# Optimization experiments

Hardware: AMD Instinct MI355X
Metric: run time of the kernel (lower is better)

The kernel has to match this reference:

```python
import jax, jax.numpy as jnp
import numpy as np


def _dsepconv(inp, vert, horiz, offx, offy, mask):
    # inp: [B,C,H,W]; vert/horiz: [B,F,H,W]; offx/offy/mask: [B,F*F,H,W]
    B, C, H, W = inp.shape
    F = vert.shape[1]
    FF = F * F
    dt = inp.dtype
    k = jnp.arange(FF)
    ki = (k // F).astype(dt)   # vertical tap index i
    kj = (k % F).astype(dt)    # horizontal tap index j
    half = jnp.asarray((F - 1) / 2.0, dt)
    ys = jnp.arange(H, dtype=dt)
    xs = jnp.arange(W, dtype=dt)
    # per-pixel deformable sample positions, [B,FF,H,W]
    py = offy + ys[None, None, :, None] + (ki - half)[None, :, None, None]
    px = offx + xs[None, None, None, :] + (kj - half)[None, :, None, None]
    py = jnp.clip(py, 0.0, H - 1)
    px = jnp.clip(px, 0.0, W - 1)
    y0f = jnp.floor(py)
    x0f = jnp.floor(px)
    wy = py - y0f   # bilinear fractional weights
    wx = px - x0f
    y0 = y0f.astype(jnp.int32)
    x0 = x0f.astype(jnp.int32)
    y1 = jnp.minimum(y0 + 1, H - 1)
    x1 = jnp.minimum(x0 + 1, W - 1)

    inp_flat = inp.reshape(B, C, H * W)

    def gather(yi, xi):
        # flat spatial gather per batch element -> [B,C,FF,H,W]
        idx = (yi * W + xi).reshape(B, FF * H * W)
        g = jax.vmap(lambda im, ix: im[:, ix])(inp_flat, idx)
        return g.reshape(B, C, FF, H, W)

    g00 = gather(y0, x0)
    g01 = gather(y0, x1)
    g10 = gather(y1, x0)
    g11 = gather(y1, x1)
    wy_ = wy[:, None]  # [B,1,FF,H,W]
    wx_ = wx[:, None]
    samp = (g00 * (1 - wy_) * (1 - wx_)
            + g01 * (1 - wy_) * wx_
            + g10 * wy_ * (1 - wx_)
            + g11 * wy_ * wx_)  # [B,C,FF,H,W]
    # separable mask-weighted tap weights: vert[i]*horiz[j]*mask[k]
    wtap = vert[:, k // F] * horiz[:, k % F] * mask  # [B,FF,H,W]
    return jnp.einsum('bkhw,bckhw->bchw', wtap, samp)


def setup_inputs() -> dict:
    key = jax.random.key(0)
    ks = jax.random.split(key, 6)
    B, C, H, W, F = 4, 3, 384, 384, 5
    return {
        'tensorInput': jax.random.normal(ks[0], (B, C, H, W), jnp.float32),
        'tensorVertical': jax.random.uniform(ks[1], (B, F, H, W), jnp.float32),
        'tensorHorizontal': jax.random.uniform(ks[2], (B, F, H, W), jnp.float32),
        'tensorOffsetX': jax.random.normal(ks[3], (B, F * F, H, W), jnp.float32),
        'tensorOffsetY': jax.random.normal(ks[4], (B, F * F, H, W), jnp.float32),
        'tensorMask': jax.random.uniform(ks[5], (B, F * F, H, W), jnp.float32),
    }


def reference(tensorInput, tensorVertical, tensorHorizontal, tensorOffsetX, tensorOffsetY, tensorMask):
    return _dsepconv(tensorInput, tensorVertical, tensorHorizontal,
                     tensorOffsetX, tensorOffsetY, tensorMask)
```

## Files before the change

### kernel.cpp

```cpp
#include <hip/hip_runtime.h>
#include <hip/hip_fp16.h>

#define BB 4
#define CC 3
#define HH 384
#define WW 384
#define FF 5
#define KK 25
#define HW (HH*WW)
#define WP 192
#define TOT (BB*HH*WP)

#define TX 64
#define TY 8

typedef float fx2 __attribute__((ext_vector_type(2)));

__device__ __forceinline__ fx2 nt_load2(const float* p) {
    return __builtin_nontemporal_load((const fx2*)p);
}

__device__ __forceinline__ uint2 pack_px(float c0, float c1, float c2) {
    __half2 h01 = __floats2half2_rn(c0, c1);
    uint2 r;
    r.x = *(const unsigned int*)&h01;
    r.y = (unsigned int)__half_as_ushort(__float2half_rn(c2));
    return r;
}

__global__ __launch_bounds__(256) void pack_kernel(
    const float* __restrict__ inp, uint4* __restrict__ tab)
{
    int t = blockIdx.x * blockDim.x + threadIdx.x;
    if (t >= TOT) return;
    int j = t % WP;
    int y = (t / WP) % HH;
    int b = t / (WP * HH);
    int p0 = 2 * j, p1 = 2 * j + 1, p2 = min(2 * j + 2, WW - 1);
    const float* b0 = inp + (((size_t)b * CC + 0) * HH + y) * WW;
    const float* b1 = inp + (((size_t)b * CC + 1) * HH + y) * WW;
    const float* b2 = inp + (((size_t)b * CC + 2) * HH + y) * WW;
    uint2 q0 = pack_px(b0[p0], b1[p0], b2[p0]);
    uint2 q1 = pack_px(b0[p1], b1[p1], b2[p1]);
    uint2 q2 = pack_px(b0[p2], b1[p2], b2[p2]);
    tab[t]       = make_uint4(q0.x, q0.y, q1.x, q1.y);
    tab[TOT + t] = make_uint4(q1.x, q1.y, q2.x, q2.y);
}

__device__ __forceinline__ void unpack_pair(uint4 r,
    float& lo0, float& lo1, float& lo2, float& hi0, float& hi1, float& hi2)
{
    float2 lo01 = __half22float2(*(const __half2*)&r.x);
    float2 hi01 = __half22float2(*(const __half2*)&r.z);
    lo0 = lo01.x; lo1 = lo01.y;
    hi0 = hi01.x; hi1 = hi01.y;
    lo2 = __half2float(*(const __half*)&r.y);
    hi2 = __half2float(*(const __half*)&r.w);
}

__global__ __launch_bounds__(256) void dsepconv_kernel(
    const uint4* __restrict__ tab,
    const float* __restrict__ vert,
    const float* __restrict__ horiz,
    const float* __restrict__ offx,
    const float* __restrict__ offy,
    const float* __restrict__ mask,
    float* __restrict__ out)
{
    int tx = threadIdx.x & 31;
    int ty = threadIdx.x >> 5;
    int xb = blockIdx.x * TX + tx * 2;
    int y  = blockIdx.y * TY + ty;
    int b  = blockIdx.z;
    int planeoff = y * WW + xb;

    fx2 v2[FF], h2[FF];
#pragma unroll
    for (int f = 0; f < FF; ++f) {
        v2[f] = nt_load2(vert  + (b * FF + f) * HW + planeoff);
        h2[f] = nt_load2(horiz + (b * FF + f) * HW + planeoff);
    }

    const uint4* tb = tab + (size_t)b * (HH * WP);

    float acc[2][3] = {{0.f,0.f,0.f},{0.f,0.f,0.f}};
    const float fy = (float)y;

    for (int ki = 0; ki < FF; ++ki) {
        float dy = fy + (float)(ki - 2);
        const float* ox_p = offx + (size_t)(b * KK + ki * FF) * HW + planeoff;
        const float* oy_p = offy + (size_t)(b * KK + ki * FF) * HW + planeoff;
        const float* m_p  = mask + (size_t)(b * KK + ki * FF) * HW + planeoff;
#pragma unroll
        for (int kj = 0; kj < FF; ++kj) {
            fx2 ox2 = nt_load2(ox_p + kj * HW);
            fx2 oy2 = nt_load2(oy_p + kj * HW);
            fx2 m2  = nt_load2(m_p  + kj * HW);
#pragma unroll
            for (int p = 0; p < 2; ++p) {
                float wt = v2[ki][p] * h2[kj][p] * m2[p];
                float py = oy2[p] + dy;
                float px = ox2[p] + (float)(xb + p + kj - 2);
                py = fminf(fmaxf(py, 0.f), (float)(HH - 1));
                px = fminf(fmaxf(px, 0.f), (float)(WW - 1));
                float y0f = floorf(py);
                float x0f = floorf(px);
                float wy = py - y0f;
                float wx = px - x0f;
                int y0 = (int)y0f;
                int x0 = (int)x0f;
                int y1 = min(y0 + 1, HH - 1);

                int j    = x0 >> 1;
                const uint4* tbs = tb + ((x0 & 1) ? TOT : 0);
                uint4 r0 = tbs[y0 * WP + j];
                uint4 r1 = tbs[y1 * WP + j];

                float a00,a01,a02,b00,b01,b02;
                float a10,a11,a12,b10,b11,b12;
                unpack_pair(r0, a00,a01,a02, b00,b01,b02);
                unpack_pair(r1, a10,a11,a12, b10,b11,b12);

                float w00 = (1.f - wy) * (1.f - wx);
                float w01 = (1.f - wy) * wx;
                float w10 = wy * (1.f - wx);
                float w11 = wy * wx;

                acc[p][0] += wt * (a00*w00 + b00*w01 + a10*w10 + b10*w11);
                acc[p][1] += wt * (a01*w00 + b01*w01 + a11*w10 + b11*w11);
                acc[p][2] += wt * (a02*w00 + b02*w01 + a12*w10 + b12*w11);
            }
        }
    }

#pragma unroll
    for (int c = 0; c < CC; ++c) {
        fx2 o; o.x = acc[0][c]; o.y = acc[1][c];
        *(fx2*)(out + ((size_t)b * CC + c) * HW + planeoff) = o;
    }
}

extern "C" void kernel_launch(void* const* d_in, const int* in_sizes, int n_in,
                              void* d_out, int out_size, void* d_ws, size_t ws_size,
                              hipStream_t stream) {
    const float* inp   = (const float*)d_in[0];
    const float* vert  = (const float*)d_in[1];
    const float* horiz = (const float*)d_in[2];
    const float* offx  = (const float*)d_in[3];
    const float* offy  = (const float*)d_in[4];
    const float* mask  = (const float*)d_in[5];
    float* out = (float*)d_out;
    uint4* tab = (uint4*)d_ws;

    {
        pack_kernel<<<(TOT + 255) / 256, 256, 0, stream>>>(inp, tab);
    }
    {
        dim3 grid(WW / TX, HH / TY, BB);
        dsepconv_kernel<<<grid, 256, 0, stream>>>(
            tab, vert, horiz, offx, offy, mask, out);
    }
}
```

Baseline: 219.3 us.

## Map one pixel per thread with fully unrolled tap loops and batched loads

```diff
diff --git a/kernel.cpp b/kernel.cpp
--- a/kernel.cpp
+++ b/kernel.cpp
@@ -12,12 +12,12 @@
 #define TOT (BB*HH*WP)
 
 #define TX 64
-#define TY 8
+#define TY 4
 
 typedef float fx2 __attribute__((ext_vector_type(2)));
 
-__device__ __forceinline__ fx2 nt_load2(const float* p) {
-    return __builtin_nontemporal_load((const fx2*)p);
+__device__ __forceinline__ float nt_load(const float* p) {
+    return __builtin_nontemporal_load(p);
 }
 
 __device__ __forceinline__ uint2 pack_px(float c0, float c1, float c2) {
@@ -36,13 +36,18 @@
     int j = t % WP;
     int y = (t / WP) % HH;
     int b = t / (WP * HH);
-    int p0 = 2 * j, p1 = 2 * j + 1, p2 = min(2 * j + 2, WW - 1);
+    int p0 = 2 * j;
+    int p2 = min(2 * j + 2, WW - 1);
     const float* b0 = inp + (((size_t)b * CC + 0) * HH + y) * WW;
     const float* b1 = inp + (((size_t)b * CC + 1) * HH + y) * WW;
     const float* b2 = inp + (((size_t)b * CC + 2) * HH + y) * WW;
-    uint2 q0 = pack_px(b0[p0], b1[p0], b2[p0]);
-    uint2 q1 = pack_px(b0[p1], b1[p1], b2[p1]);
-    uint2 q2 = pack_px(b0[p2], b1[p2], b2[p2]);
+    fx2 a0 = *(const fx2*)(b0 + p0);
+    fx2 a1 = *(const fx2*)(b1 + p0);
+    fx2 a2 = *(const fx2*)(b2 + p0);
+    float c0 = b0[p2], c1 = b1[p2], c2 = b2[p2];
+    uint2 q0 = pack_px(a0.x, a1.x, a2.x);
+    uint2 q1 = pack_px(a0.y, a1.y, a2.y);
+    uint2 q2 = pack_px(c0, c1, c2);
     tab[t]       = make_uint4(q0.x, q0.y, q1.x, q1.y);
     tab[TOT + t] = make_uint4(q1.x, q1.y, q2.x, q2.y);
 }
@@ -58,7 +63,7 @@
     hi2 = __half2float(*(const __half*)&r.w);
 }
 
-__global__ __launch_bounds__(256) void dsepconv_kernel(
+__global__ __launch_bounds__(256, 6) void dsepconv_kernel(
     const uint4* __restrict__ tab,
     const float* __restrict__ vert,
     const float* __restrict__ horiz,
@@ -67,77 +72,79 @@
     const float* __restrict__ mask,
     float* __restrict__ out)
 {
-    int tx = threadIdx.x & 31;
-    int ty = threadIdx.x >> 5;
-    int xb = blockIdx.x * TX + tx * 2;
+    int tx = threadIdx.x & 63;
+    int ty = threadIdx.x >> 6;
+    int x  = blockIdx.x * TX + tx;
     int y  = blockIdx.y * TY + ty;
     int b  = blockIdx.z;
-    int planeoff = y * WW + xb;
+    int planeoff = y * WW + x;
 
-    fx2 v2[FF], h2[FF];
+    float v[FF], h[FF];
 #pragma unroll
     for (int f = 0; f < FF; ++f) {
-        v2[f] = nt_load2(vert  + (b * FF + f) * HW + planeoff);
-        h2[f] = nt_load2(horiz + (b * FF + f) * HW + planeoff);
+        v[f] = nt_load(vert  + (b * FF + f) * HW + planeoff);
+        h[f] = nt_load(horiz + (b * FF + f) * HW + planeoff);
     }
 
     const uint4* tb = tab + (size_t)b * (HH * WP);
 
-    float acc[2][3] = {{0.f,0.f,0.f},{0.f,0.f,0.f}};
+    float acc0 = 0.f, acc1 = 0.f, acc2 = 0.f;
     const float fy = (float)y;
 
+#pragma unroll
     for (int ki = 0; ki < FF; ++ki) {
-        float dy = fy + (float)(ki - 2);
+        const float dy = fy + (float)(ki - 2);
         const float* ox_p = offx + (size_t)(b * KK + ki * FF) * HW + planeoff;
         const float* oy_p = offy + (size_t)(b * KK + ki * FF) * HW + planeoff;
         const float* m_p  = mask + (size_t)(b * KK + ki * FF) * HW + planeoff;
+
+        float oxv[FF], oyv[FF], mv[FF];
 #pragma unroll
         for (int kj = 0; kj < FF; ++kj) {
-            fx2 ox2 = nt_load2(ox_p + kj * HW);
-            fx2 oy2 = nt_load2(oy_p + kj * HW);
-            fx2 m2  = nt_load2(m_p  + kj * HW);
+            oxv[kj] = nt_load(ox_p + kj * HW);
+            oyv[kj] = nt_load(oy_p + kj * HW);
+            mv[kj]  = nt_load(m_p  + kj * HW);
+        }
+
 #pragma unroll
-            for (int p = 0; p < 2; ++p) {
-                float wt = v2[ki][p] * h2[kj][p] * m2[p];
-                float py = oy2[p] + dy;
-                float px = ox2[p] + (float)(xb + p + kj - 2);
-                py = fminf(fmaxf(py, 0.f), (float)(HH - 1));
-                px = fminf(fmaxf(px, 0.f), (float)(WW - 1));
-                float y0f = floorf(py);
-                float x0f = floorf(px);
-                float wy = py - y0f;
-                float wx = px - x0f;
-                int y0 = (int)y0f;
-                int x0 = (int)x0f;
-                int y1 = min(y0 + 1, HH - 1);
+        for (int kj = 0; kj < FF; ++kj) {
+            float wt = v[ki] * h[kj] * mv[kj];
+            float py = oyv[kj] + dy;
+            float px = oxv[kj] + (float)(x + kj - 2);
+            py = fminf(fmaxf(py, 0.f), (float)(HH - 1));
+            px = fminf(fmaxf(px, 0.f), (float)(WW - 1));
+            float y0f = floorf(py);
+            float x0f = floorf(px);
+            float wy = py - y0f;
+            float wx = px - x0f;
+            int y0 = (int)y0f;
+            int x0 = (int)x0f;
+            int y1 = min(y0 + 1, HH - 1);
 
-                int j    = x0 >> 1;
-                const uint4* tbs = tb + ((x0 & 1) ? TOT : 0);
-                uint4 r0 = tbs[y0 * WP + j];
-                uint4 r1 = tbs[y1 * WP + j];
+            int j    = x0 >> 1;
+            const uint4* tbs = tb + ((x0 & 1) ? TOT : 0);
+            uint4 r0 = tbs[y0 * WP + j];
+            uint4 r1 = tbs[y1 * WP + j];
 
-                float a00,a01,a02,b00,b01,b02;
-                float a10,a11,a12,b10,b11,b12;
-                unpack_pair(r0, a00,a01,a02, b00,b01,b02);
-                unpack_pair(r1, a10,a11,a12, b10,b11,b12);
+            float a00,a01,a02,b00,b01,b02;
+            float a10,a11,a12,b10,b11,b12;
+            unpack_pair(r0, a00,a01,a02, b00,b01,b02);
+            unpack_pair(r1, a10,a11,a12, b10,b11,b12);
 
-                float w00 = (1.f - wy) * (1.f - wx);
-                float w01 = (1.f - wy) * wx;
-                float w10 = wy * (1.f - wx);
-                float w11 = wy * wx;
+            float w00 = (1.f - wy) * (1.f - wx);
+            float w01 = (1.f - wy) * wx;
+            float w10 = wy * (1.f - wx);
+            float w11 = wy * wx;
 
-                acc[p][0] += wt * (a00*w00 + b00*w01 + a10*w10 + b10*w11);
-                acc[p][1] += wt * (a01*w00 + b01*w01 + a11*w10 + b11*w11);
-                acc[p][2] += wt * (a02*w00 + b02*w01 + a12*w10 + b12*w11);
-            }
+            acc0 += wt * (a00*w00 + b00*w01 + a10*w10 + b10*w11);
+            acc1 += wt * (a01*w00 + b01*w01 + a11*w10 + b11*w11);
+            acc2 += wt * (a02*w00 + b02*w01 + a12*w10 + b12*w11);
         }
     }
 
-#pragma unroll
-    for (int c = 0; c < CC; ++c) {
-        fx2 o; o.x = acc[0][c]; o.y = acc[1][c];
-        *(fx2*)(out + ((size_t)b * CC + c) * HW + planeoff) = o;
-    }
+    out[((size_t)b * CC + 0) * HW + planeoff] = acc0;
+    out[((size_t)b * CC + 1) * HW + planeoff] = acc1;
+    out[((size_t)b * CC + 2) * HW + planeoff] = acc2;
 }
 
 extern "C" void kernel_launch(void* const* d_in, const int* in_sizes, int n_in,
```

Result: slower. 236.2 us (+7.7%).

## Stage input tile with halo in LDS and drop separate pack kernel

Applied to the files above, without the earlier changes.

```diff
diff --git a/kernel.cpp b/kernel.cpp
--- a/kernel.cpp
+++ b/kernel.cpp
@@ -8,11 +8,13 @@
 #define FF 5
 #define KK 25
 #define HW (HH*WW)
-#define WP 192
-#define TOT (BB*HH*WP)
 
 #define TX 64
 #define TY 8
+#define MARG 8
+#define RH (TY + 2*MARG + 1)
+#define RW (TX + 2*MARG)
+#define SMN (RH*RW)
 
 typedef float fx2 __attribute__((ext_vector_type(2)));
 
@@ -28,38 +30,14 @@
     return r;
 }
 
-__global__ __launch_bounds__(256) void pack_kernel(
-    const float* __restrict__ inp, uint4* __restrict__ tab)
-{
-    int t = blockIdx.x * blockDim.x + threadIdx.x;
-    if (t >= TOT) return;
-    int j = t % WP;
-    int y = (t / WP) % HH;
-    int b = t / (WP * HH);
-    int p0 = 2 * j, p1 = 2 * j + 1, p2 = min(2 * j + 2, WW - 1);
-    const float* b0 = inp + (((size_t)b * CC + 0) * HH + y) * WW;
-    const float* b1 = inp + (((size_t)b * CC + 1) * HH + y) * WW;
-    const float* b2 = inp + (((size_t)b * CC + 2) * HH + y) * WW;
-    uint2 q0 = pack_px(b0[p0], b1[p0], b2[p0]);
-    uint2 q1 = pack_px(b0[p1], b1[p1], b2[p1]);
-    uint2 q2 = pack_px(b0[p2], b1[p2], b2[p2]);
-    tab[t]       = make_uint4(q0.x, q0.y, q1.x, q1.y);
-    tab[TOT + t] = make_uint4(q1.x, q1.y, q2.x, q2.y);
-}
-
-__device__ __forceinline__ void unpack_pair(uint4 r,
-    float& lo0, float& lo1, float& lo2, float& hi0, float& hi1, float& hi2)
-{
-    float2 lo01 = __half22float2(*(const __half2*)&r.x);
-    float2 hi01 = __half22float2(*(const __half2*)&r.z);
-    lo0 = lo01.x; lo1 = lo01.y;
-    hi0 = hi01.x; hi1 = hi01.y;
-    lo2 = __half2float(*(const __half*)&r.y);
-    hi2 = __half2float(*(const __half*)&r.w);
+__device__ __forceinline__ void unpack_px(uint2 r, float& c0, float& c1, float& c2) {
+    float2 f01 = __half22float2(*(const __half2*)&r.x);
+    c0 = f01.x; c1 = f01.y;
+    c2 = __half2float(*(const __half*)&r.y);
 }
 
 __global__ __launch_bounds__(256) void dsepconv_kernel(
-    const uint4* __restrict__ tab,
+    const float* __restrict__ inp,
     const float* __restrict__ vert,
     const float* __restrict__ horiz,
     const float* __restrict__ offx,
@@ -67,12 +45,31 @@
     const float* __restrict__ mask,
     float* __restrict__ out)
 {
+    __shared__ uint2 smem[SMN];
+
     int tx = threadIdx.x & 31;
     int ty = threadIdx.x >> 5;
-    int xb = blockIdx.x * TX + tx * 2;
-    int y  = blockIdx.y * TY + ty;
+    int X  = blockIdx.x * TX;
+    int Y  = blockIdx.y * TY;
+    int xb = X + tx * 2;
+    int y  = Y + ty;
     int b  = blockIdx.z;
+    int ylo = Y - MARG, xlo = X - MARG;
     int planeoff = y * WW + xb;
+
+    const float* c0p = inp + ((size_t)b * CC + 0) * HW;
+    const float* c1p = inp + ((size_t)b * CC + 1) * HW;
+    const float* c2p = inp + ((size_t)b * CC + 2) * HW;
+
+    for (int p = threadIdx.x; p < SMN; p += 256) {
+        int r = p / RW;
+        int c = p - r * RW;
+        int gy = min(max(ylo + r, 0), HH - 1);
+        int gx = min(max(xlo + c, 0), WW - 1);
+        int o  = gy * WW + gx;
+        smem[p] = pack_px(c0p[o], c1p[o], c2p[o]);
+    }
+    __syncthreads();
 
     fx2 v2[FF], h2[FF];
 #pragma unroll
@@ -80,8 +77,6 @@
         v2[f] = nt_load2(vert  + (b * FF + f) * HW + planeoff);
         h2[f] = nt_load2(horiz + (b * FF + f) * HW + planeoff);
     }
-
-    const uint4* tb = tab + (size_t)b * (HH * WP);
 
     float acc[2][3] = {{0.f,0.f,0.f},{0.f,0.f,0.f}};
     const float fy = (float)y;
@@ -109,26 +104,45 @@
                 float wx = px - x0f;
                 int y0 = (int)y0f;
                 int x0 = (int)x0f;
-                int y1 = min(y0 + 1, HH - 1);
 
-                int j    = x0 >> 1;
-                const uint4* tbs = tb + ((x0 & 1) ? TOT : 0);
-                uint4 r0 = tbs[y0 * WP + j];
-                uint4 r1 = tbs[y1 * WP + j];
+                int y0r = y0 - ylo;
+                int x0r = x0 - xlo;
+                bool ok = ((unsigned)y0r <= (unsigned)(RH - 2)) &
+                          ((unsigned)x0r <= (unsigned)(RW - 2));
 
-                float a00,a01,a02,b00,b01,b02;
-                float a10,a11,a12,b10,b11,b12;
-                unpack_pair(r0, a00,a01,a02, b00,b01,b02);
-                unpack_pair(r1, a10,a11,a12, b10,b11,b12);
+                float s00c0,s00c1,s00c2, s01c0,s01c1,s01c2;
+                float s10c0,s10c1,s10c2, s11c0,s11c1,s11c2;
+                if (ok) {
+                    int dxo = (x0 < WW - 1) ? 1 : 0;
+                    int dyo = (y0 < HH - 1) ? RW : 0;
+                    int a   = y0r * RW + x0r;
+                    uint2 r00 = smem[a];
+                    uint2 r01 = smem[a + dxo];
+                    uint2 r10 = smem[a + dyo];
+                    uint2 r11 = smem[a + dyo + dxo];
+                    unpack_px(r00, s00c0, s00c1, s00c2);
+                    unpack_px(r01, s01c0, s01c1, s01c2);
+                    unpack_px(r10, s10c0, s10c1, s10c2);
+                    unpack_px(r11, s11c0, s11c1, s11c2);
+                } else {
+                    int x1 = min(x0 + 1, WW - 1);
+                    int y1 = min(y0 + 1, HH - 1);
+                    int o00 = y0 * WW + x0, o01 = y0 * WW + x1;
+                    int o10 = y1 * WW + x0, o11 = y1 * WW + x1;
+                    s00c0 = c0p[o00]; s00c1 = c1p[o00]; s00c2 = c2p[o00];
+                    s01c0 = c0p[o01]; s01c1 = c1p[o01]; s01c2 = c2p[o01];
+                    s10c0 = c0p[o10]; s10c1 = c1p[o10]; s10c2 = c2p[o10];
+                    s11c0 = c0p[o11]; s11c1 = c1p[o11]; s11c2 = c2p[o11];
+                }
 
                 float w00 = (1.f - wy) * (1.f - wx);
                 float w01 = (1.f - wy) * wx;
                 float w10 = wy * (1.f - wx);
                 float w11 = wy * wx;
 
-                acc[p][0] += wt * (a00*w00 + b00*w01 + a10*w10 + b10*w11);
-                acc[p][1] += wt * (a01*w00 + b01*w01 + a11*w10 + b11*w11);
-                acc[p][2] += wt * (a02*w00 + b02*w01 + a12*w10 + b12*w11);
+                acc[p][0] += wt * (s00c0*w00 + s01c0*w01 + s10c0*w10 + s11c0*w11);
+                acc[p][1] += wt * (s00c1*w00 + s01c1*w01 + s10c1*w10 + s11c1*w11);
+                acc[p][2] += wt * (s00c2*w00 + s01c2*w01 + s10c2*w10 + s11c2*w11);
             }
         }
     }
@@ -150,14 +164,8 @@
     const float* offy  = (const float*)d_in[4];
     const float* mask  = (const float*)d_in[5];
     float* out = (float*)d_out;
-    uint4* tab = (uint4*)d_ws;
 
-    {
-        pack_kernel<<<(TOT + 255) / 256, 256, 0, stream>>>(inp, tab);
-    }
-    {
-        dim3 grid(WW / TX, HH / TY, BB);
-        dsepconv_kernel<<<grid, 256, 0, stream>>>(
-            tab, vert, horiz, offx, offy, mask, out);
-    }
+    dim3 grid(WW / TX, HH / TY, BB);
+    dsepconv_kernel<<<grid, 256, 0, stream>>>(
+        inp, vert, horiz, offx, offy, mask, out);
 }
```

Result: slower. 254.8 us (+16.2%).

## Software-pipeline offset/mask loads and shrink blocks to one wavefront

Applied to the files above, without the earlier changes.

```diff
diff --git a/kernel.cpp b/kernel.cpp
--- a/kernel.cpp
+++ b/kernel.cpp
@@ -12,7 +12,7 @@
 #define TOT (BB*HH*WP)
 
 #define TX 64
-#define TY 8
+#define TY 2
 
 typedef float fx2 __attribute__((ext_vector_type(2)));
 
@@ -36,13 +36,18 @@
     int j = t % WP;
     int y = (t / WP) % HH;
     int b = t / (WP * HH);
-    int p0 = 2 * j, p1 = 2 * j + 1, p2 = min(2 * j + 2, WW - 1);
+    int p0 = 2 * j;
+    int p2 = min(2 * j + 2, WW - 1);
     const float* b0 = inp + (((size_t)b * CC + 0) * HH + y) * WW;
     const float* b1 = inp + (((size_t)b * CC + 1) * HH + y) * WW;
     const float* b2 = inp + (((size_t)b * CC + 2) * HH + y) * WW;
-    uint2 q0 = pack_px(b0[p0], b1[p0], b2[p0]);
-    uint2 q1 = pack_px(b0[p1], b1[p1], b2[p1]);
-    uint2 q2 = pack_px(b0[p2], b1[p2], b2[p2]);
+    fx2 a0 = *(const fx2*)(b0 + p0);
+    fx2 a1 = *(const fx2*)(b1 + p0);
+    fx2 a2 = *(const fx2*)(b2 + p0);
+    float c0 = b0[p2], c1 = b1[p2], c2 = b2[p2];
+    uint2 q0 = pack_px(a0.x, a1.x, a2.x);
+    uint2 q1 = pack_px(a0.y, a1.y, a2.y);
+    uint2 q2 = pack_px(c0, c1, c2);
     tab[t]       = make_uint4(q0.x, q0.y, q1.x, q1.y);
     tab[TOT + t] = make_uint4(q1.x, q1.y, q2.x, q2.y);
 }
@@ -58,7 +63,7 @@
     hi2 = __half2float(*(const __half*)&r.w);
 }
 
-__global__ __launch_bounds__(256) void dsepconv_kernel(
+__global__ __launch_bounds__(64) void dsepconv_kernel(
     const uint4* __restrict__ tab,
     const float* __restrict__ vert,
     const float* __restrict__ horiz,
@@ -82,20 +87,38 @@
     }
 
     const uint4* tb = tab + (size_t)b * (HH * WP);
+    const float* ox_base = offx + (size_t)b * KK * HW + planeoff;
+    const float* oy_base = offy + (size_t)b * KK * HW + planeoff;
+    const float* m_base  = mask + (size_t)b * KK * HW + planeoff;
 
     float acc[2][3] = {{0.f,0.f,0.f},{0.f,0.f,0.f}};
     const float fy = (float)y;
 
+    fx2 oxb[2][FF], oyb[2][FF], mb[2][FF];
+#pragma unroll
+    for (int kj = 0; kj < FF; ++kj) {
+        oxb[0][kj] = nt_load2(ox_base + kj * HW);
+        oyb[0][kj] = nt_load2(oy_base + kj * HW);
+        mb[0][kj]  = nt_load2(m_base  + kj * HW);
+    }
+
+#pragma unroll
     for (int ki = 0; ki < FF; ++ki) {
-        float dy = fy + (float)(ki - 2);
-        const float* ox_p = offx + (size_t)(b * KK + ki * FF) * HW + planeoff;
-        const float* oy_p = offy + (size_t)(b * KK + ki * FF) * HW + planeoff;
-        const float* m_p  = mask + (size_t)(b * KK + ki * FF) * HW + planeoff;
+        const int cur = ki & 1, nxt = cur ^ 1;
+        if (ki + 1 < FF) {
+#pragma unroll
+            for (int kj = 0; kj < FF; ++kj) {
+                oxb[nxt][kj] = nt_load2(ox_base + ((ki+1) * FF + kj) * HW);
+                oyb[nxt][kj] = nt_load2(oy_base + ((ki+1) * FF + kj) * HW);
+                mb[nxt][kj]  = nt_load2(m_base  + ((ki+1) * FF + kj) * HW);
+            }
+        }
+        const float dy = fy + (float)(ki - 2);
 #pragma unroll
         for (int kj = 0; kj < FF; ++kj) {
-            fx2 ox2 = nt_load2(ox_p + kj * HW);
-            fx2 oy2 = nt_load2(oy_p + kj * HW);
-            fx2 m2  = nt_load2(m_p  + kj * HW);
+            fx2 ox2 = oxb[cur][kj];
+            fx2 oy2 = oyb[cur][kj];
+            fx2 m2  = mb[cur][kj];
 #pragma unroll
             for (int p = 0; p < 2; ++p) {
                 float wt = v2[ki][p] * h2[kj][p] * m2[p];
@@ -157,7 +180,7 @@
     }
     {
         dim3 grid(WW / TX, HH / TY, BB);
-        dsepconv_kernel<<<grid, 256, 0, stream>>>(
+        dsepconv_kernel<<<grid, 64, 0, stream>>>(
             tab, vert, horiz, offx, offy, mask, out);
     }
 }
```

After: 269.7 us. +23.0%, slower.
